# Optimization experiments

Measured on AMD Instinct MI355X. Metric: run time of the kernel, lower is better.

Reference implementation:

```python
import jax, jax.numpy as jnp
import numpy as np

N, E = 50000, 800000
IN, OUT, STEPS = 100, 200, 8
CAT = IN + OUT  # 300
EPS = 1e-5


def setup_inputs() -> dict:
    key = jax.random.key(0)
    ks = jax.random.split(key, 24)
    s = 0.05
    d = {}
    d["x"] = jax.random.normal(ks[0], (N, IN), jnp.float32)
    d["edge_index"] = jax.random.randint(ks[1], (2, E), 0, N, dtype=jnp.int32)
    # GatedGraphConv params: per-layer linear weight + shared GRUCell
    d["ggnn_w"] = jax.random.normal(ks[2], (STEPS, OUT, OUT), jnp.float32) * s
    d["gru_wih"] = jax.random.normal(ks[3], (3 * OUT, OUT), jnp.float32) * s
    d["gru_whh"] = jax.random.normal(ks[4], (3 * OUT, OUT), jnp.float32) * s
    d["gru_bih"] = jnp.zeros((3 * OUT,), jnp.float32)
    d["gru_bhh"] = jnp.zeros((3 * OUT,), jnp.float32)
    # conv branch on h_i (C=OUT)
    d["conv1_w"] = jax.random.normal(ks[5], (OUT, OUT, 4), jnp.float32) * s
    d["conv1_b"] = jnp.zeros((OUT,), jnp.float32)
    d["conv2_w"] = jax.random.normal(ks[6], (OUT, OUT, 2), jnp.float32) * s
    d["conv2_b"] = jnp.zeros((OUT,), jnp.float32)
    # conv branch on c_i (C=CAT)
    d["conv1c_w"] = jax.random.normal(ks[7], (CAT, CAT, 4), jnp.float32) * s
    d["conv1c_b"] = jnp.zeros((CAT,), jnp.float32)
    d["conv2c_w"] = jax.random.normal(ks[8], (CAT, CAT, 2), jnp.float32) * s
    d["conv2c_b"] = jnp.zeros((CAT,), jnp.float32)
    # batchnorms (training-mode batch stats; affine params)
    d["bn_g"] = jnp.ones((OUT,), jnp.float32)
    d["bn_b"] = jnp.zeros((OUT,), jnp.float32)
    d["bnc_g"] = jnp.ones((CAT,), jnp.float32)
    d["bnc_b"] = jnp.zeros((CAT,), jnp.float32)
    # output MLPs
    d["mlpy_w"] = jax.random.normal(ks[9], (2, OUT), jnp.float32) * s
    d["mlpy_b"] = jnp.zeros((2,), jnp.float32)
    d["mlpz_w"] = jax.random.normal(ks[10], (2, CAT), jnp.float32) * s
    d["mlpz_b"] = jnp.zeros((2,), jnp.float32)
    return d


def _batchnorm(x, g, b):  # x: [B, C, L], stats over (B, L) as in BN1d training
    mu = x.mean(axis=(0, 2), keepdims=True)
    var = ((x - mu) ** 2).mean(axis=(0, 2), keepdims=True)
    return (x - mu) / jnp.sqrt(var + EPS) * g[None, :, None] + b[None, :, None]


def _conv1d(x, w, b):  # x: [B, C, L], w: [O, I, K]
    y = jax.lax.conv_general_dilated(x, w, (1,), 'VALID',
                                     dimension_numbers=('NCH', 'OIH', 'NCH'))
    return y + b[None, :, None]


def _maxpool1d(x, k, s):  # x: [B, C, L]
    return jax.lax.reduce_window(x, -jnp.inf, jax.lax.max,
                                 (1, 1, k), (1, 1, s), 'VALID')


def _ggnn(x, edge_index, ggnn_w, gru_wih, gru_whh, gru_bih, gru_bhh):
    # PyG GatedGraphConv: pad features to out_channels, then per layer:
    # m = h @ W_l; agg[dst] += m[src]; h = GRUCell(agg, h)
    h = jnp.pad(x, ((0, 0), (0, OUT - IN)))  # [N, OUT]
    src, dst = edge_index[0], edge_index[1]

    def step(h, w):
        m = h @ w                                               # [N, OUT]
        agg = jax.ops.segment_sum(m[src], dst, num_segments=N)  # scatter-add
        gi = agg @ gru_wih.T + gru_bih
        gh = h @ gru_whh.T + gru_bhh
        ir, iz, ic = jnp.split(gi, 3, axis=1)
        hr, hz, hc = jnp.split(gh, 3, axis=1)
        r = jax.nn.sigmoid(ir + hr)
        z = jax.nn.sigmoid(iz + hz)
        n = jnp.tanh(ic + r * hc)
        return (1.0 - z) * n + z * h, None

    h, _ = jax.lax.scan(step, h, ggnn_w)
    return h


def reference(x, edge_index, ggnn_w, gru_wih, gru_whh, gru_bih, gru_bhh,
              conv1_w, conv1_b, conv2_w, conv2_b,
              conv1c_w, conv1c_b, conv2c_w, conv2c_b,
              bn_g, bn_b, bnc_g, bnc_b,
              mlpy_w, mlpy_b, mlpz_w, mlpz_b):
    h = _ggnn(x, edge_index, ggnn_w, gru_wih, gru_whh, gru_bih, gru_bhh)
    x_i = x[None]                      # [1, N, IN]
    h_i = h[None]                      # [1, N, OUT]
    c_i = jnp.concatenate([h_i, x_i], axis=-1)  # [1, N, CAT]

    y = jnp.transpose(h_i, (0, 2, 1))  # [1, OUT, N]
    y = _maxpool1d(jax.nn.relu(_batchnorm(_conv1d(y, conv1_w, conv1_b), bn_g, bn_b)), 4, 2)
    y = _maxpool1d(jax.nn.relu(_batchnorm(_conv1d(y, conv2_w, conv2_b), bn_g, bn_b)), 3, 2)
    Y2 = jnp.transpose(y, (0, 2, 1))   # [1, L2, OUT]

    zc = jnp.transpose(c_i, (0, 2, 1))  # [1, CAT, N]
    zc = _maxpool1d(jax.nn.relu(_batchnorm(_conv1d(zc, conv1c_w, conv1c_b), bnc_g, bnc_b)), 4, 2)
    zc = _maxpool1d(jax.nn.relu(_batchnorm(_conv1d(zc, conv2c_w, conv2c_b), bnc_g, bnc_b)), 3, 2)
    Z2 = jnp.transpose(zc, (0, 2, 1))  # [1, L2, CAT]

    before_avg = (Y2 @ mlpy_w.T + mlpy_b) * (Z2 @ mlpz_w.T + mlpz_b)  # [1, L2, 2]
    avg = before_avg.mean(axis=1)      # [1, 2]
    return jax.nn.softmax(avg, axis=-1)
```

## Files before the change

kernel.cpp:

```cpp
#include <hip/hip_runtime.h>
#include <cstdint>
#include <cstddef>

#define NNODES 50000
#define NEDGES 800000
#define FIN    100
#define FOUT   200
#define FCAT   300
#define NSTEPS 8
#define NSCANB 196

typedef unsigned short ushort_t;
typedef __bf16 bf16x8 __attribute__((ext_vector_type(8)));
typedef float  floatx4 __attribute__((ext_vector_type(4)));

__device__ __forceinline__ float bf2f(ushort_t u) {
  union { unsigned u; float f; } c; c.u = ((unsigned)u) << 16; return c.f;
}
__device__ __forceinline__ ushort_t f2bf(float f) {
  union { float f; unsigned u; } c; c.f = f;
  unsigned r = c.u + 0x7FFFu + ((c.u >> 16) & 1u);
  return (ushort_t)(r >> 16);
}
__device__ __forceinline__ float inval(const void* p, size_t i, int f32) {
  return f32 ? ((const float*)p)[i] : bf2f(((const ushort_t*)p)[i]);
}

__device__ __forceinline__ void gl2lds16(const ushort_t* g, ushort_t* l) {
  typedef const __attribute__((address_space(1))) unsigned int gu32;
  typedef __attribute__((address_space(3))) unsigned int lu32;
  __builtin_amdgcn_global_load_lds((gu32*)(uintptr_t)g, (lu32*)(uintptr_t)l, 16, 0, 0);
}

#define LOG2E 1.44269504f
__device__ __forceinline__ float fsigmoid(float x) {
  return __builtin_amdgcn_rcpf(1.f + __builtin_amdgcn_exp2f(-x * LOG2E));
}
__device__ __forceinline__ float ftanh(float a) {
  return 1.f - 2.f * __builtin_amdgcn_rcpf(1.f + __builtin_amdgcn_exp2f(2.f * LOG2E * a));
}

__global__ void probe_kernel(const void* xraw, int* flag) {
  const ushort_t* u = (const ushort_t*)xraw;
  int t = threadIdx.x;
  int bad = 0;
  for (int i = t; i < 2048; i += 64) {
    int e = (u[2 * i] >> 7) & 0xFF;
    if (e >= 0x88) bad++;
  }
  for (int off = 32; off; off >>= 1) bad += __shfl_down(bad, off);
  if (t == 0) *flag = (bad > 128) ? 1 : 0;
}

__global__ void zero_kernel(int* p, int n) {
  int i = blockIdx.x * 256 + threadIdx.x;
  if (i < n) p[i] = 0;
}

__global__ void sentinel_kernel(ushort_t* out) {
  if (threadIdx.x == 0 && blockIdx.x == 0) {
    out[0] = f2bf(0.123f);
    out[1] = f2bf(0.877f);
  }
}

__global__ void hinit_kernel(const void* __restrict__ x, const int* __restrict__ dflag,
                             ushort_t* __restrict__ h) {
  const int f32 = *dflag;
  int i = blockIdx.x * 256 + threadIdx.x;
  if (i >= NNODES * FOUT) return;
  int n = i / FOUT, c = i % FOUT;
  h[i] = (c < FIN) ? f2bf(inval(x, (size_t)n * FIN + c, f32)) : (ushort_t)0;
}

__global__ void ccat_kernel(const ushort_t* __restrict__ h, const void* __restrict__ x,
                            const int* __restrict__ dflag, ushort_t* __restrict__ cc) {
  const int f32 = *dflag;
  int i = blockIdx.x * 256 + threadIdx.x;
  if (i >= NNODES * FCAT) return;
  int n = i / FCAT, c = i % FCAT;
  cc[i] = (c < FOUT) ? h[n * FOUT + c] : f2bf(inval(x, (size_t)n * FIN + (c - FOUT), f32));
}

__global__ void hist_kernel(const int* __restrict__ dst, int* __restrict__ cnt) {
  int e = blockIdx.x * 256 + threadIdx.x;
  if (e < NEDGES) atomicAdd(&cnt[dst[e]], 1);
}

__global__ void bsum_kernel(const int* __restrict__ cnt, int* __restrict__ bsum) {
  __shared__ int red[4];
  int i = blockIdx.x * 256 + threadIdx.x;
  int v = (i < NNODES) ? cnt[i] : 0;
  for (int off = 32; off; off >>= 1) v += __shfl_down(v, off);
  int w = threadIdx.x >> 6;
  if ((threadIdx.x & 63) == 0) red[w] = v;
  __syncthreads();
  if (threadIdx.x == 0) bsum[blockIdx.x] = red[0] + red[1] + red[2] + red[3];
}

__global__ void bscan_kernel(const int* __restrict__ bsum, int* __restrict__ boff) {
  __shared__ int s[256];
  int t = threadIdx.x;
  int v = (t < NSCANB) ? bsum[t] : 0;
  s[t] = v;
  __syncthreads();
  for (int off = 1; off < 256; off <<= 1) {
    int u = (t >= off) ? s[t - off] : 0;
    __syncthreads();
    s[t] += u;
    __syncthreads();
  }
  if (t < NSCANB) boff[t] = s[t] - v;
}

__global__ void rowptr_kernel(const int* __restrict__ cnt, const int* __restrict__ boff,
                              int* __restrict__ row_ptr, int* __restrict__ cursor) {
  __shared__ int s[256];
  int t = threadIdx.x;
  int i = blockIdx.x * 256 + t;
  int v = (i < NNODES) ? cnt[i] : 0;
  s[t] = v;
  __syncthreads();
  for (int off = 1; off < 256; off <<= 1) {
    int u = (t >= off) ? s[t - off] : 0;
    __syncthreads();
    s[t] += u;
    __syncthreads();
  }
  if (i < NNODES) {
    int e = boff[blockIdx.x] + s[t] - v;
    row_ptr[i] = e; cursor[i] = e;
    if (i == NNODES - 1) row_ptr[NNODES] = boff[blockIdx.x] + s[t];
  }
}

__global__ void fill_kernel(const int* __restrict__ srcv, const int* __restrict__ dstv,
                            int* __restrict__ cursor, int* __restrict__ csr_src) {
  int e = blockIdx.x * 256 + threadIdx.x;
  if (e >= NEDGES) return;
  int p = atomicAdd(&cursor[dstv[e]], 1);
  csr_src[p] = srcv[e];
}

__global__ __launch_bounds__(256) void gather_kernel(
    const int* __restrict__ row_ptr, const int* __restrict__ csr_src,
    const ushort_t* __restrict__ h, ushort_t* __restrict__ Ag) {
  int g = threadIdx.x >> 6;
  int lane = threadIdx.x & 63;
  int n = blockIdx.x * 4 + g;
  if (n >= NNODES) return;
  if (lane >= 50) return;
  int s0 = row_ptr[n], s1 = row_ptr[n + 1];
  float a0 = 0.f, a1 = 0.f, a2 = 0.f, a3 = 0.f;
  int i = s0;
  for (; i + 3 < s1; i += 4) {
    int sa = csr_src[i], sb = csr_src[i + 1], sc = csr_src[i + 2], sd = csr_src[i + 3];
    ushort4 va = *(const ushort4*)&h[(size_t)sa * FOUT + lane * 4];
    ushort4 vb = *(const ushort4*)&h[(size_t)sb * FOUT + lane * 4];
    ushort4 vc = *(const ushort4*)&h[(size_t)sc * FOUT + lane * 4];
    ushort4 vd = *(const ushort4*)&h[(size_t)sd * FOUT + lane * 4];
    a0 += (bf2f(va.x) + bf2f(vb.x)) + (bf2f(vc.x) + bf2f(vd.x));
    a1 += (bf2f(va.y) + bf2f(vb.y)) + (bf2f(vc.y) + bf2f(vd.y));
    a2 += (bf2f(va.z) + bf2f(vb.z)) + (bf2f(vc.z) + bf2f(vd.z));
    a3 += (bf2f(va.w) + bf2f(vb.w)) + (bf2f(vc.w) + bf2f(vd.w));
  }
  for (; i < s1; i++) {
    int sa = csr_src[i];
    ushort4 va = *(const ushort4*)&h[(size_t)sa * FOUT + lane * 4];
    a0 += bf2f(va.x); a1 += bf2f(va.y); a2 += bf2f(va.z); a3 += bf2f(va.w);
  }
  ushort4 o;
  o.x = f2bf(a0); o.y = f2bf(a1); o.z = f2bf(a2); o.w = f2bf(a3);
  *(ushort4*)&Ag[(size_t)n * 400 + lane * 4] = o;
  *(ushort4*)&Ag[(size_t)n * 400 + FOUT + lane * 4] =
      *(const ushort4*)&h[(size_t)n * FOUT + lane * 4];
}

__global__ void pada_kernel(const void* __restrict__ src, const int* __restrict__ dflag,
                            ushort_t* __restrict__ dst, int K, int Kp, int rowsValid,
                            int total) {
  const int f32 = *dflag;
  int i = blockIdx.x * 256 + threadIdx.x;
  if (i >= total) return;
  int r = i / Kp, k = i % Kp;
  float v = (r < rowsValid && k < K) ? inval(src, (size_t)r * K + k, f32) : 0.f;
  dst[i] = f2bf(v);
}

__global__ void btgruq_kernel(const float* __restrict__ Wp, const void* __restrict__ whh,
                              const int* __restrict__ dflag, ushort_t* __restrict__ Bt) {
  const int f32 = *dflag;
  int i = blockIdx.x * 256 + threadIdx.x;
  if (i >= NSTEPS * 896 * 416) return;
  int l = i / (896 * 416);
  int rem = i % (896 * 416);
  int nn = rem / 416;
  int k = rem % 416;
  int c = nn >> 2, g = nn & 3;
  float v = 0.f;
  if (c < 200) {
    if (k < 200) {
      const float* wrow = Wp + ((size_t)l * 200 + k) * 600;
      if (g == 0) v = wrow[c];
      else if (g == 1) v = wrow[200 + c];
      else if (g == 2) v = wrow[400 + c];
    } else if (k < 400) {
      int kh = k - 200;
      if (g == 0) v = inval(whh, (size_t)c * 200 + kh, f32);
      else if (g == 1) v = inval(whh, (size_t)(200 + c) * 200 + kh, f32);
      else if (g == 3) v = inval(whh, (size_t)(400 + c) * 200 + kh, f32);
    }
  }
  Bt[((size_t)nn + 896 * (size_t)l) * 416 + k] = f2bf(v);
}

__global__ void btconv_kernel(const void* __restrict__ w, const int* __restrict__ dflag,
                              ushort_t* __restrict__ Bt, int C, int KT, int Kp,
                              int O, int total) {
  const int f32 = *dflag;
  int i = blockIdx.x * 256 + threadIdx.x;
  if (i >= total) return;
  int o = i / Kp, k = i % Kp;
  float v = 0.f;
  int K = C * KT;
  if (k < K && o < O) {
    int ktap = k / C; int ci = k % C;
    v = inval(w, ((size_t)o * C + ci) * KT + ktap, f32);
  }
  Bt[i] = f2bf(v);
}

__global__ void gbias_kernel(const void* __restrict__ bih, const void* __restrict__ bhh,
                             const int* __restrict__ dflag, float* __restrict__ gb) {
  const int f32 = *dflag;
  int c = blockIdx.x * 256 + threadIdx.x;
  if (c >= 200) return;
  gb[c]       = inval(bih, c, f32)       + inval(bhh, c, f32);
  gb[200 + c] = inval(bih, 200 + c, f32) + inval(bhh, 200 + c, f32);
  gb[400 + c] = inval(bih, 400 + c, f32);
  gb[600 + c] = inval(bhh, 400 + c, f32);
}

__device__ __forceinline__ bool xcd_tile(int id, int MT, int NT, int& mt, int& nt) {
  int xcd = id & 7;
  int slot = id >> 3;
  mt = xcd * ((MT + 7) >> 3) + slot / NT;
  nt = slot % NT;
  return mt < MT;
}

template <bool OUT_BF16>
__global__ __launch_bounds__(256) void gemm128(
    const ushort_t* __restrict__ A, int lda, const ushort_t* __restrict__ Bt,
    void* __restrict__ Cv, int ldc, int M, int N, int Kp,
    const float* __restrict__ bias) {
  __shared__ alignas(16) ushort_t As[128 * 32];
  __shared__ alignas(16) ushort_t Bs[128 * 32];
  const int MT = (M + 127) >> 7;
  const int NT = (N + 127) >> 7;
  int mt, nt;
  if (!xcd_tile(blockIdx.x, MT, NT, mt, nt)) return;
  const int m0 = mt * 128;
  const int n0 = nt * 128;
  const int tid = threadIdx.x;
  const int lane = tid & 63;
  const int wv = tid >> 6;
  const int wm = wv & 1;
  const int wn = wv >> 1;
  const int quad = lane >> 4;
  const int l15 = lane & 15;

  const int s0i = wv * 128 + lane;
  const int s1i = s0i + 64;
  const int r0 = s0i >> 2, c0 = (s0i & 3) ^ ((r0 >> 1) & 3);
  const int r1 = s1i >> 2, c1 = (s1i & 3) ^ ((r1 >> 1) & 3);
  int ar0 = m0 + r0; if (ar0 >= M) ar0 = M - 1;
  int ar1 = m0 + r1; if (ar1 >= M) ar1 = M - 1;
  const ushort_t* gA0 = A + (size_t)ar0 * lda + c0 * 8;
  const ushort_t* gA1 = A + (size_t)ar1 * lda + c1 * 8;
  const ushort_t* gB0 = Bt + (size_t)(n0 + r0) * Kp + c0 * 8;
  const ushort_t* gB1 = Bt + (size_t)(n0 + r1) * Kp + c1 * 8;
  ushort_t* lA0 = &As[(size_t)(wv * 128) * 8];
  ushort_t* lA1 = &As[(size_t)(wv * 128 + 64) * 8];
  ushort_t* lB0 = &Bs[(size_t)(wv * 128) * 8];
  ushort_t* lB1 = &Bs[(size_t)(wv * 128 + 64) * 8];

  floatx4 acc[4][4];
  #pragma unroll
  for (int a = 0; a < 4; a++)
    #pragma unroll
    for (int b = 0; b < 4; b++)
      acc[a][b] = (floatx4){0.f, 0.f, 0.f, 0.f};

  for (int k0 = 0; k0 < Kp; k0 += 32) {
    gl2lds16(gA0 + k0, lA0);
    gl2lds16(gA1 + k0, lA1);
    gl2lds16(gB0 + k0, lB0);
    gl2lds16(gB1 + k0, lB1);
    __syncthreads();
    bf16x8 af[4], bfr[4];
    #pragma unroll
    for (int t = 0; t < 4; t++) {
      int ra = wm * 64 + t * 16 + l15;
      int rb = wn * 64 + t * 16 + l15;
      af[t]  = *(const bf16x8*)&As[(ra * 4 + (quad ^ ((ra >> 1) & 3))) * 8];
      bfr[t] = *(const bf16x8*)&Bs[(rb * 4 + (quad ^ ((rb >> 1) & 3))) * 8];
    }
    #pragma unroll
    for (int tm = 0; tm < 4; tm++)
      #pragma unroll
      for (int tn = 0; tn < 4; tn++)
        acc[tm][tn] = __builtin_amdgcn_mfma_f32_16x16x32_bf16(af[tm], bfr[tn], acc[tm][tn], 0, 0, 0);
    __syncthreads();
  }

  #pragma unroll
  for (int tm = 0; tm < 4; tm++) {
    int row = m0 + wm * 64 + tm * 16 + quad * 4;
    #pragma unroll
    for (int tn = 0; tn < 4; tn++) {
      int col = n0 + wn * 64 + tn * 16 + l15;
      if (col < N) {
        float bb = bias ? bias[col] : 0.f;
        #pragma unroll
        for (int r = 0; r < 4; r++) {
          if (row + r < M) {
            float v = acc[tm][tn][r] + bb;
            if (OUT_BF16) ((ushort_t*)Cv)[(size_t)(row + r) * ldc + col] = f2bf(v);
            else          ((float*)Cv)[(size_t)(row + r) * ldc + col] = v;
          }
        }
      }
    }
  }
}

__global__ __launch_bounds__(256) void gemm_gru(
    const ushort_t* __restrict__ A, int lda, const ushort_t* __restrict__ Bt,
    ushort_t* __restrict__ h, int M, int Kp, const float* __restrict__ gb) {
  __shared__ alignas(16) ushort_t As[128 * 32];
  __shared__ alignas(16) ushort_t Bs[128 * 32];
  const int MT = (M + 127) >> 7;
  int mt, nt;
  if (!xcd_tile(blockIdx.x, MT, 7, mt, nt)) return;
  const int m0 = mt * 128;
  const int n0 = nt * 128;
  const int tid = threadIdx.x;
  const int lane = tid & 63;
  const int wv = tid >> 6;
  const int wm = wv & 1;
  const int wn = wv >> 1;
  const int quad = lane >> 4;
  const int l15 = lane & 15;

  const int s0i = wv * 128 + lane;
  const int s1i = s0i + 64;
  const int r0 = s0i >> 2, c0 = (s0i & 3) ^ ((r0 >> 1) & 3);
  const int r1 = s1i >> 2, c1 = (s1i & 3) ^ ((r1 >> 1) & 3);
  int ar0 = m0 + r0; if (ar0 >= M) ar0 = M - 1;
  int ar1 = m0 + r1; if (ar1 >= M) ar1 = M - 1;
  const ushort_t* gA0 = A + (size_t)ar0 * lda + c0 * 8;
  const ushort_t* gA1 = A + (size_t)ar1 * lda + c1 * 8;
  const ushort_t* gB0 = Bt + (size_t)(n0 + r0) * Kp + c0 * 8;
  const ushort_t* gB1 = Bt + (size_t)(n0 + r1) * Kp + c1 * 8;
  ushort_t* lA0 = &As[(size_t)(wv * 128) * 8];
  ushort_t* lA1 = &As[(size_t)(wv * 128 + 64) * 8];
  ushort_t* lB0 = &Bs[(size_t)(wv * 128) * 8];
  ushort_t* lB1 = &Bs[(size_t)(wv * 128 + 64) * 8];

  floatx4 acc[4][4];
  #pragma unroll
  for (int a = 0; a < 4; a++)
    #pragma unroll
    for (int b = 0; b < 4; b++)
      acc[a][b] = (floatx4){0.f, 0.f, 0.f, 0.f};

  for (int k0 = 0; k0 < Kp; k0 += 32) {
    gl2lds16(gA0 + k0, lA0);
    gl2lds16(gA1 + k0, lA1);
    gl2lds16(gB0 + k0, lB0);
    gl2lds16(gB1 + k0, lB1);
    __syncthreads();
    bf16x8 af[4], bfr[4];
    #pragma unroll
    for (int t = 0; t < 4; t++) {
      int ra = wm * 64 + t * 16 + l15;
      int rb = wn * 64 + t * 16 + l15;
      af[t]  = *(const bf16x8*)&As[(ra * 4 + (quad ^ ((ra >> 1) & 3))) * 8];
      bfr[t] = *(const bf16x8*)&Bs[(rb * 4 + (quad ^ ((rb >> 1) & 3))) * 8];
    }
    #pragma unroll
    for (int tm = 0; tm < 4; tm++)
      #pragma unroll
      for (int tn = 0; tn < 4; tn++)
        acc[tm][tn] = __builtin_amdgcn_mfma_f32_16x16x32_bf16(af[tm], bfr[tn], acc[tm][tn], 0, 0, 0);
    __syncthreads();
  }

  const int sb0 = l15 & 1;
  const int sb1 = (l15 >> 1) & 1;
  const int jch = l15 >> 2;
  const int chb = nt * 32 + wn * 16;
  #pragma unroll
  for (int tn = 0; tn < 4; tn++) {
    int chan = chb + tn * 4 + jch;
    bool chok = (chan < 200);
    float rb = 0.f, zb = 0.f, ib = 0.f, hb = 0.f;
    if (chok) {
      rb = gb[chan]; zb = gb[200 + chan]; ib = gb[400 + chan]; hb = gb[600 + chan];
    }
    #pragma unroll
    for (int tm = 0; tm < 4; tm++) {
      float v0 = acc[tm][tn][0], v1 = acc[tm][tn][1];
      float v2 = acc[tm][tn][2], v3 = acc[tm][tn][3];
      float t;
      t = __shfl_xor(sb0 ? v0 : v1, 1); if (sb0) v0 = t; else v1 = t;
      t = __shfl_xor(sb0 ? v2 : v3, 1); if (sb0) v2 = t; else v3 = t;
      t = __shfl_xor(sb1 ? v0 : v2, 2); if (sb1) v0 = t; else v2 = t;
      t = __shfl_xor(sb1 ? v1 : v3, 2); if (sb1) v1 = t; else v3 = t;
      int row = m0 + wm * 64 + tm * 16 + quad * 4 + (l15 & 3);
      if (row < M && chok) {
        float r_ = fsigmoid(v0 + rb);
        float z_ = fsigmoid(v1 + zb);
        float n_ = ftanh(v2 + ib + r_ * (v3 + hb));
        float ho = bf2f(h[(size_t)row * 200 + chan]);
        h[(size_t)row * 200 + chan] = f2bf((1.f - z_) * n_ + z_ * ho);
      }
    }
  }
}

__global__ void bias_kernel(const void* __restrict__ b, const int* __restrict__ dflag,
                            float* __restrict__ out, int n) {
  const int f32 = *dflag;
  int i = blockIdx.x * 256 + threadIdx.x;
  if (i < n) out[i] = inval(b, i, f32);
}

__global__ void stats_kernel(const float* __restrict__ X, int Lrows, int C,
                             float* __restrict__ sums, float* __restrict__ sumsq) {
  int r0 = blockIdx.x * 64;
  int rend = r0 + 64; if (rend > Lrows) rend = Lrows;
  for (int c = threadIdx.x; c < C; c += 256) {
    float s = 0.f, ss = 0.f;
    for (int r = r0; r < rend; r++) {
      float v = X[(size_t)r * C + c];
      s += v; ss += v * v;
    }
    atomicAdd(&sums[c], s);
    atomicAdd(&sumsq[c], ss);
  }
}

__global__ void bnpool_kernel(const float* __restrict__ X, int Lin, int C, int kk, int ss,
                              int Lp, const float* __restrict__ sums,
                              const float* __restrict__ sumsq,
                              const void* __restrict__ g, const void* __restrict__ b,
                              const int* __restrict__ dflag, ushort_t* __restrict__ out) {
  const int f32 = *dflag;
  int i = blockIdx.x * 256 + threadIdx.x;
  if (i >= Lp * C) return;
  int p = i / C, c = i % C;
  float inv = 1.f / (float)Lin;
  float mu = sums[c] * inv;
  float var = sumsq[c] * inv - mu * mu; if (var < 0.f) var = 0.f;
  float scale = inval(g, c, f32) * rsqrtf(var + 1e-5f);
  float shift = inval(b, c, f32) - mu * scale;
  float m = -1e30f;
  int base = p * ss;
  for (int r = 0; r < kk; r++) {
    float v = X[(size_t)(base + r) * C + c] * scale + shift;
    if (v > m) m = v;
  }
  if (m < 0.f) m = 0.f;
  out[(size_t)p * C + c] = f2bf(m);
}

__global__ __launch_bounds__(256) void final_kernel(
    const ushort_t* __restrict__ Y2, const ushort_t* __restrict__ Z2,
    const void* __restrict__ wy, const void* __restrict__ by,
    const void* __restrict__ wz, const void* __restrict__ bz,
    const int* __restrict__ dflag, float* __restrict__ pacc) {
  const int f32 = *dflag;
  __shared__ float bl[8];
  int g = threadIdx.x >> 6;
  int lane = threadIdx.x & 63;
  int row = blockIdx.x * 4 + g;
  float y0 = 0.f, y1 = 0.f, z0 = 0.f, z1 = 0.f;
  if (row < 12497) {
    for (int c = lane; c < 200; c += 64) {
      float v = bf2f(Y2[(size_t)row * 200 + c]);
      y0 += v * inval(wy, c, f32);
      y1 += v * inval(wy, 200 + c, f32);
    }
    for (int c = lane; c < 300; c += 64) {
      float v = bf2f(Z2[(size_t)row * 300 + c]);
      z0 += v * inval(wz, c, f32);
      z1 += v * inval(wz, 300 + c, f32);
    }
  }
  for (int off = 32; off > 0; off >>= 1) {
    y0 += __shfl_down(y0, off);
    y1 += __shfl_down(y1, off);
    z0 += __shfl_down(z0, off);
    z1 += __shfl_down(z1, off);
  }
  if (lane == 0) {
    float p0 = 0.f, p1 = 0.f;
    if (row < 12497) {
      p0 = (y0 + inval(by, 0, f32)) * (z0 + inval(bz, 0, f32));
      p1 = (y1 + inval(by, 1, f32)) * (z1 + inval(bz, 1, f32));
    }
    bl[g * 2] = p0; bl[g * 2 + 1] = p1;
  }
  __syncthreads();
  if (threadIdx.x == 0) {
    pacc[(size_t)blockIdx.x * 2]     = bl[0] + bl[2] + bl[4] + bl[6];
    pacc[(size_t)blockIdx.x * 2 + 1] = bl[1] + bl[3] + bl[5] + bl[7];
  }
}

__global__ __launch_bounds__(256) void finalize_kernel(
    const float* __restrict__ pacc, int nblk, const int* __restrict__ dflag,
    void* __restrict__ out) {
  const int f32 = *dflag;
  __shared__ float red[2][4];
  int t = threadIdx.x;
  float s0 = 0.f, s1 = 0.f;
  for (int i = t; i < nblk; i += 256) { s0 += pacc[2 * i]; s1 += pacc[2 * i + 1]; }
  for (int off = 32; off; off >>= 1) { s0 += __shfl_down(s0, off); s1 += __shfl_down(s1, off); }
  int w = t >> 6;
  if ((t & 63) == 0) { red[0][w] = s0; red[1][w] = s1; }
  __syncthreads();
  if (t == 0) {
    float a0 = (red[0][0] + red[0][1] + red[0][2] + red[0][3]) / 12497.f;
    float a1 = (red[1][0] + red[1][1] + red[1][2] + red[1][3]) / 12497.f;
    float mx = fmaxf(a0, a1);
    float e0 = expf(a0 - mx), e1 = expf(a1 - mx);
    float s = e0 + e1;
    if (f32) {
      ((float*)out)[0] = e0 / s;
      ((float*)out)[1] = e1 / s;
    } else {
      ((ushort_t*)out)[0] = f2bf(e0 / s);
      ((ushort_t*)out)[1] = f2bf(e1 / s);
    }
  }
}

static inline int xcd_grid(int M, int NT) {
  int MT = (M + 127) >> 7;
  int CH = (MT + 7) >> 3;
  return 8 * CH * NT;
}

extern "C" void kernel_launch(void* const* d_in, const int* in_sizes, int n_in,
                              void* d_out, int out_size, void* d_ws, size_t ws_size,
                              hipStream_t stream) {
  const void* x        = d_in[0];
  const int*  edge     = (const int*)d_in[1];
  const void* ggnn_w   = d_in[2];
  const void* gru_wih  = d_in[3];
  const void* gru_whh  = d_in[4];
  const void* gru_bih  = d_in[5];
  const void* gru_bhh  = d_in[6];
  const void* conv1_w  = d_in[7];
  const void* conv1_b  = d_in[8];
  const void* conv2_w  = d_in[9];
  const void* conv2_b  = d_in[10];
  const void* conv1c_w = d_in[11];
  const void* conv1c_b = d_in[12];
  const void* conv2c_w = d_in[13];
  const void* conv2c_b = d_in[14];
  const void* bn_g     = d_in[15];
  const void* bn_b     = d_in[16];
  const void* bnc_g    = d_in[17];
  const void* bnc_b    = d_in[18];
  const void* mlpy_w   = d_in[19];
  const void* mlpy_b   = d_in[20];
  const void* mlpz_w   = d_in[21];
  const void* mlpz_b   = d_in[22];
  const int* srcv = edge;
  const int* dstv = edge + NEDGES;

  char* p = (char*)d_ws;
  auto alloc = [&](size_t bytes) -> char* {
    char* r = p; p += (bytes + 255) & ~(size_t)255; return r;
  };
  ushort_t* h    = (ushort_t*)alloc(((size_t)NNODES * FOUT + 64) * 2);
  ushort_t* Ag   = (ushort_t*)alloc(((size_t)NNODES * 400 + 64) * 2);
  ushort_t* cc   = Ag;
  char*     R    = alloc((size_t)98 * 1000 * 1000);
  float*    C1   = (float*)R;
  float*    C2   = (float*)R;
  float*    C1c  = (float*)R;
  float*    C2c  = (float*)R;
  ushort_t* pooled1 = (ushort_t*)(R + 60000000);
  ushort_t* pooledc = (ushort_t*)(R + 70000000);
  ushort_t* Y2      = (ushort_t*)(R + 85000000);
  ushort_t* Z2      = (ushort_t*)(R + 90000000);
  ushort_t* BtG  = (ushort_t*)alloc((size_t)8 * 896 * 416 * 2);
  ushort_t* Bt1  = (ushort_t*)alloc((size_t)256 * 800 * 2);
  ushort_t* Bt2  = (ushort_t*)alloc((size_t)256 * 416 * 2);
  ushort_t* Bt1c = (ushort_t*)alloc((size_t)384 * 1216 * 2);
  ushort_t* Bt2c = (ushort_t*)alloc((size_t)384 * 608 * 2);
  ushort_t* gwp  = (ushort_t*)alloc((size_t)1600 * 224 * 2);
  ushort_t* wihp = (ushort_t*)alloc((size_t)640 * 224 * 2);
  float*    Wp   = (float*)alloc((size_t)1600 * 600 * 4);
  int*   csr_src = (int*)alloc((size_t)NEDGES * 4);
  int*   row_ptr = (int*)alloc((size_t)(NNODES + 1) * 4);
  int*   cursor  = (int*)alloc((size_t)NNODES * 4);
  int*   cnt     = (int*)alloc((size_t)NNODES * 4);
  int*   bsum    = (int*)alloc((size_t)(NSCANB + 4) * 4);
  int*   boff    = (int*)alloc((size_t)(NSCANB + 4) * 4);
  float* pacc    = (float*)alloc((size_t)3125 * 2 * 4);
  float* sb      = (float*)alloc((size_t)4300 * 4);
  float *s1 = sb, *ss1 = sb + 200, *s2 = sb + 400, *ss2 = sb + 600;
  float *sc1 = sb + 800, *ssc1 = sb + 1100, *sc2 = sb + 1400, *ssc2 = sb + 1700;
  int*   dflag = (int*)(sb + 2002);
  float* b1f   = sb + 2010;
  float* b2f   = sb + 2210;
  float* b1cf  = sb + 2410;
  float* b2cf  = sb + 2710;
  float* gb    = sb + 3100;

  size_t required = (size_t)(p - (char*)d_ws);
  if (required > ws_size) {
    sentinel_kernel<<<1, 64, 0, stream>>>((ushort_t*)d_out);
    return;
  }

  probe_kernel<<<1, 64, 0, stream>>>(x, dflag);
  zero_kernel<<<(NNODES + 255) / 256, 256, 0, stream>>>(cnt, NNODES);
  zero_kernel<<<(2000 + 255) / 256, 256, 0, stream>>>((int*)sb, 2000);
  hinit_kernel<<<(NNODES * FOUT + 255) / 256, 256, 0, stream>>>(x, dflag, h);

  pada_kernel<<<(1600 * 224 + 255) / 256, 256, 0, stream>>>(ggnn_w, dflag, gwp, 200, 224, 1600, 1600 * 224);
  pada_kernel<<<(640 * 224 + 255) / 256, 256, 0, stream>>>(gru_wih, dflag, wihp, 200, 224, 600, 640 * 224);
  gemm128<false><<<xcd_grid(1600, 5), 256, 0, stream>>>(gwp, 224, wihp, Wp, 600, 1600, 600, 224, nullptr);

  btgruq_kernel<<<(NSTEPS * 896 * 416 + 255) / 256, 256, 0, stream>>>(Wp, gru_whh, dflag, BtG);
  gbias_kernel<<<1, 256, 0, stream>>>(gru_bih, gru_bhh, dflag, gb);
  btconv_kernel<<<(256 * 800 + 255) / 256, 256, 0, stream>>>(conv1_w, dflag, Bt1, 200, 4, 800, 200, 256 * 800);
  btconv_kernel<<<(256 * 416 + 255) / 256, 256, 0, stream>>>(conv2_w, dflag, Bt2, 200, 2, 416, 200, 256 * 416);
  btconv_kernel<<<(384 * 1216 + 255) / 256, 256, 0, stream>>>(conv1c_w, dflag, Bt1c, 300, 4, 1216, 300, 384 * 1216);
  btconv_kernel<<<(384 * 608 + 255) / 256, 256, 0, stream>>>(conv2c_w, dflag, Bt2c, 300, 2, 608, 300, 384 * 608);
  bias_kernel<<<1, 256, 0, stream>>>(conv1_b, dflag, b1f, 200);
  bias_kernel<<<1, 256, 0, stream>>>(conv2_b, dflag, b2f, 200);
  bias_kernel<<<2, 256, 0, stream>>>(conv1c_b, dflag, b1cf, 300);
  bias_kernel<<<2, 256, 0, stream>>>(conv2c_b, dflag, b2cf, 300);

  hist_kernel<<<(NEDGES + 255) / 256, 256, 0, stream>>>(dstv, cnt);
  bsum_kernel<<<NSCANB, 256, 0, stream>>>(cnt, bsum);
  bscan_kernel<<<1, 256, 0, stream>>>(bsum, boff);
  rowptr_kernel<<<NSCANB, 256, 0, stream>>>(cnt, boff, row_ptr, cursor);
  fill_kernel<<<(NEDGES + 255) / 256, 256, 0, stream>>>(srcv, dstv, cursor, csr_src);

  for (int l = 0; l < NSTEPS; l++) {
    gather_kernel<<<(NNODES + 3) / 4, 256, 0, stream>>>(row_ptr, csr_src, h, Ag);
    gemm_gru<<<xcd_grid(NNODES, 7), 256, 0, stream>>>(Ag, 400, BtG + (size_t)l * 896 * 416,
                                                      h, NNODES, 416, gb);
  }
  ccat_kernel<<<(NNODES * FCAT + 255) / 256, 256, 0, stream>>>(h, x, dflag, cc);

  gemm128<false><<<xcd_grid(49997, 2), 256, 0, stream>>>(h, 200, Bt1, C1, 200, 49997, 200, 800, b1f);
  stats_kernel<<<(49997 + 63) / 64, 256, 0, stream>>>(C1, 49997, 200, s1, ss1);
  bnpool_kernel<<<(24997 * 200 + 255) / 256, 256, 0, stream>>>(C1, 49997, 200, 4, 2, 24997,
                                                               s1, ss1, bn_g, bn_b, dflag, pooled1);
  gemm128<false><<<xcd_grid(24996, 2), 256, 0, stream>>>(pooled1, 200, Bt2, C2, 200, 24996, 200, 416, b2f);
  stats_kernel<<<(24996 + 63) / 64, 256, 0, stream>>>(C2, 24996, 200, s2, ss2);
  bnpool_kernel<<<(12497 * 200 + 255) / 256, 256, 0, stream>>>(C2, 24996, 200, 3, 2, 12497,
                                                               s2, ss2, bn_g, bn_b, dflag, Y2);
  gemm128<false><<<xcd_grid(49997, 3), 256, 0, stream>>>(cc, 300, Bt1c, C1c, 300, 49997, 300, 1216, b1cf);
  stats_kernel<<<(49997 + 63) / 64, 256, 0, stream>>>(C1c, 49997, 300, sc1, ssc1);
  bnpool_kernel<<<(24997 * 300 + 255) / 256, 256, 0, stream>>>(C1c, 49997, 300, 4, 2, 24997,
                                                               sc1, ssc1, bnc_g, bnc_b, dflag, pooledc);
  gemm128<false><<<xcd_grid(24996, 3), 256, 0, stream>>>(pooledc, 300, Bt2c, C2c, 300, 24996, 300, 608, b2cf);
  stats_kernel<<<(24996 + 63) / 64, 256, 0, stream>>>(C2c, 24996, 300, sc2, ssc2);
  bnpool_kernel<<<(12497 * 300 + 255) / 256, 256, 0, stream>>>(C2c, 24996, 300, 3, 2, 12497,
                                                               sc2, ssc2, bnc_g, bnc_b, dflag, Z2);

  final_kernel<<<3125, 256, 0, stream>>>(Y2, Z2, mlpy_w, mlpy_b, mlpz_w, mlpz_b, dflag, pacc);
  finalize_kernel<<<1, 256, 0, stream>>>(pacc, 3125, dflag, d_out);
}
```

Before: 1.797 ms.

## Fuse BN statistics into conv GEMM epilogue and drop h copy in gather

```diff
diff --git a/kernel.cpp b/kernel.cpp
--- a/kernel.cpp
+++ b/kernel.cpp
@@ -144,7 +144,7 @@
 
 __global__ __launch_bounds__(256) void gather_kernel(
     const int* __restrict__ row_ptr, const int* __restrict__ csr_src,
-    const ushort_t* __restrict__ h, ushort_t* __restrict__ Ag) {
+    const ushort_t* __restrict__ h, ushort_t* __restrict__ agg) {
   int g = threadIdx.x >> 6;
   int lane = threadIdx.x & 63;
   int n = blockIdx.x * 4 + g;
@@ -171,9 +171,7 @@
   }
   ushort4 o;
   o.x = f2bf(a0); o.y = f2bf(a1); o.z = f2bf(a2); o.w = f2bf(a3);
-  *(ushort4*)&Ag[(size_t)n * 400 + lane * 4] = o;
-  *(ushort4*)&Ag[(size_t)n * 400 + FOUT + lane * 4] =
-      *(const ushort4*)&h[(size_t)n * FOUT + lane * 4];
+  *(ushort4*)&agg[(size_t)n * 224 + lane * 4] = o;
 }
 
 __global__ void pada_kernel(const void* __restrict__ src, const int* __restrict__ dflag,
@@ -191,11 +189,11 @@
                               const int* __restrict__ dflag, ushort_t* __restrict__ Bt) {
   const int f32 = *dflag;
   int i = blockIdx.x * 256 + threadIdx.x;
-  if (i >= NSTEPS * 896 * 416) return;
-  int l = i / (896 * 416);
-  int rem = i % (896 * 416);
-  int nn = rem / 416;
-  int k = rem % 416;
+  if (i >= NSTEPS * 896 * 448) return;
+  int l = i / (896 * 448);
+  int rem = i % (896 * 448);
+  int nn = rem / 448;
+  int k = rem % 448;
   int c = nn >> 2, g = nn & 3;
   float v = 0.f;
   if (c < 200) {
@@ -204,14 +202,14 @@
       if (g == 0) v = wrow[c];
       else if (g == 1) v = wrow[200 + c];
       else if (g == 2) v = wrow[400 + c];
-    } else if (k < 400) {
-      int kh = k - 200;
+    } else if (k >= 224 && k < 424) {
+      int kh = k - 224;
       if (g == 0) v = inval(whh, (size_t)c * 200 + kh, f32);
       else if (g == 1) v = inval(whh, (size_t)(200 + c) * 200 + kh, f32);
       else if (g == 3) v = inval(whh, (size_t)(400 + c) * 200 + kh, f32);
     }
   }
-  Bt[((size_t)nn + 896 * (size_t)l) * 416 + k] = f2bf(v);
+  Bt[((size_t)nn + 896 * (size_t)l) * 448 + k] = f2bf(v);
 }
 
 __global__ void btconv_kernel(const void* __restrict__ w, const int* __restrict__ dflag,
@@ -335,9 +333,128 @@
   }
 }
 
+__global__ __launch_bounds__(256) void gemm_conv(
+    const ushort_t* __restrict__ A, int lda, const ushort_t* __restrict__ Bt,
+    ushort_t* __restrict__ C, int ldc, int M, int N, int Kp,
+    const float* __restrict__ bias, float* __restrict__ partS, float* __restrict__ partQ) {
+  __shared__ alignas(16) ushort_t As[128 * 32];
+  __shared__ alignas(16) ushort_t Bs[128 * 32];
+  const int MT = (M + 127) >> 7;
+  const int NT = (N + 127) >> 7;
+  int mt, nt;
+  if (!xcd_tile(blockIdx.x, MT, NT, mt, nt)) return;
+  const int m0 = mt * 128;
+  const int n0 = nt * 128;
+  const int tid = threadIdx.x;
+  const int lane = tid & 63;
+  const int wv = tid >> 6;
+  const int wm = wv & 1;
+  const int wn = wv >> 1;
+  const int quad = lane >> 4;
+  const int l15 = lane & 15;
+
+  const int s0i = wv * 128 + lane;
+  const int s1i = s0i + 64;
+  const int r0 = s0i >> 2, c0 = (s0i & 3) ^ ((r0 >> 1) & 3);
+  const int r1 = s1i >> 2, c1 = (s1i & 3) ^ ((r1 >> 1) & 3);
+  int ar0 = m0 + r0; if (ar0 >= M) ar0 = M - 1;
+  int ar1 = m0 + r1; if (ar1 >= M) ar1 = M - 1;
+  const ushort_t* gA0 = A + (size_t)ar0 * lda + c0 * 8;
+  const ushort_t* gA1 = A + (size_t)ar1 * lda + c1 * 8;
+  const ushort_t* gB0 = Bt + (size_t)(n0 + r0) * Kp + c0 * 8;
+  const ushort_t* gB1 = Bt + (size_t)(n0 + r1) * Kp + c1 * 8;
+  ushort_t* lA0 = &As[(size_t)(wv * 128) * 8];
+  ushort_t* lA1 = &As[(size_t)(wv * 128 + 64) * 8];
+  ushort_t* lB0 = &Bs[(size_t)(wv * 128) * 8];
+  ushort_t* lB1 = &Bs[(size_t)(wv * 128 + 64) * 8];
+
+  floatx4 acc[4][4];
+  #pragma unroll
+  for (int a = 0; a < 4; a++)
+    #pragma unroll
+    for (int b = 0; b < 4; b++)
+      acc[a][b] = (floatx4){0.f, 0.f, 0.f, 0.f};
+
+  for (int k0 = 0; k0 < Kp; k0 += 32) {
+    gl2lds16(gA0 + k0, lA0);
+    gl2lds16(gA1 + k0, lA1);
+    gl2lds16(gB0 + k0, lB0);
+    gl2lds16(gB1 + k0, lB1);
+    __syncthreads();
+    bf16x8 af[4], bfr[4];
+    #pragma unroll
+    for (int t = 0; t < 4; t++) {
+      int ra = wm * 64 + t * 16 + l15;
+      int rb = wn * 64 + t * 16 + l15;
+      af[t]  = *(const bf16x8*)&As[(ra * 4 + (quad ^ ((ra >> 1) & 3))) * 8];
+      bfr[t] = *(const bf16x8*)&Bs[(rb * 4 + (quad ^ ((rb >> 1) & 3))) * 8];
+    }
+    #pragma unroll
+    for (int tm = 0; tm < 4; tm++)
+      #pragma unroll
+      for (int tn = 0; tn < 4; tn++)
+        acc[tm][tn] = __builtin_amdgcn_mfma_f32_16x16x32_bf16(af[tm], bfr[tn], acc[tm][tn], 0, 0, 0);
+    __syncthreads();
+  }
+
+  float sS[4], sQ[4];
+  #pragma unroll
+  for (int tn = 0; tn < 4; tn++) {
+    int col = n0 + wn * 64 + tn * 16 + l15;
+    float bb = (col < N) ? bias[col] : 0.f;
+    float s = 0.f, q = 0.f;
+    #pragma unroll
+    for (int tm = 0; tm < 4; tm++) {
+      int row = m0 + wm * 64 + tm * 16 + quad * 4;
+      #pragma unroll
+      for (int r = 0; r < 4; r++) {
+        if (row + r < M) {
+          float v = acc[tm][tn][r] + bb;
+          if (col < N) C[(size_t)(row + r) * ldc + col] = f2bf(v);
+          s += v; q += v * v;
+        }
+      }
+    }
+    s += __shfl_down(s, 32); s += __shfl_down(s, 16);
+    q += __shfl_down(q, 32); q += __shfl_down(q, 16);
+    sS[tn] = s; sQ[tn] = q;
+  }
+  float* pS = (float*)As;
+  float* pQ = (float*)Bs;
+  if (quad == 0) {
+    #pragma unroll
+    for (int tn = 0; tn < 4; tn++) {
+      pS[wv * 64 + tn * 16 + l15] = sS[tn];
+      pQ[wv * 64 + tn * 16 + l15] = sQ[tn];
+    }
+  }
+  __syncthreads();
+  if (tid < 128) {
+    int wnc = tid >> 6, off = tid & 63;
+    int col = n0 + tid;
+    if (col < N) {
+      partS[(size_t)mt * N + col] = pS[(2 * wnc) * 64 + off] + pS[(2 * wnc + 1) * 64 + off];
+      partQ[(size_t)mt * N + col] = pQ[(2 * wnc) * 64 + off] + pQ[(2 * wnc + 1) * 64 + off];
+    }
+  }
+}
+
+__global__ void statred_kernel(const float* __restrict__ partS, const float* __restrict__ partQ,
+                               int MT, int N, float* __restrict__ sums, float* __restrict__ sumsq) {
+  int c = blockIdx.x * 256 + threadIdx.x;
+  if (c >= N) return;
+  float s = 0.f, q = 0.f;
+  for (int m = 0; m < MT; m++) {
+    s += partS[(size_t)m * N + c];
+    q += partQ[(size_t)m * N + c];
+  }
+  sums[c] = s; sumsq[c] = q;
+}
+
 __global__ __launch_bounds__(256) void gemm_gru(
-    const ushort_t* __restrict__ A, int lda, const ushort_t* __restrict__ Bt,
-    ushort_t* __restrict__ h, int M, int Kp, const float* __restrict__ gb) {
+    const ushort_t* __restrict__ agg, const ushort_t* __restrict__ hin,
+    const ushort_t* __restrict__ Bt, ushort_t* __restrict__ hout,
+    int M, const float* __restrict__ gb) {
   __shared__ alignas(16) ushort_t As[128 * 32];
   __shared__ alignas(16) ushort_t Bs[128 * 32];
   const int MT = (M + 127) >> 7;
@@ -359,10 +476,12 @@
   const int r1 = s1i >> 2, c1 = (s1i & 3) ^ ((r1 >> 1) & 3);
   int ar0 = m0 + r0; if (ar0 >= M) ar0 = M - 1;
   int ar1 = m0 + r1; if (ar1 >= M) ar1 = M - 1;
-  const ushort_t* gA0 = A + (size_t)ar0 * lda + c0 * 8;
-  const ushort_t* gA1 = A + (size_t)ar1 * lda + c1 * 8;
-  const ushort_t* gB0 = Bt + (size_t)(n0 + r0) * Kp + c0 * 8;
-  const ushort_t* gB1 = Bt + (size_t)(n0 + r1) * Kp + c1 * 8;
+  const ushort_t* gAg0 = agg + (size_t)ar0 * 224 + c0 * 8;
+  const ushort_t* gAg1 = agg + (size_t)ar1 * 224 + c1 * 8;
+  const ushort_t* gAh0 = hin + (size_t)ar0 * 200 + c0 * 8;
+  const ushort_t* gAh1 = hin + (size_t)ar1 * 200 + c1 * 8;
+  const ushort_t* gB0 = Bt + (size_t)(n0 + r0) * 448 + c0 * 8;
+  const ushort_t* gB1 = Bt + (size_t)(n0 + r1) * 448 + c1 * 8;
   ushort_t* lA0 = &As[(size_t)(wv * 128) * 8];
   ushort_t* lA1 = &As[(size_t)(wv * 128 + 64) * 8];
   ushort_t* lB0 = &Bs[(size_t)(wv * 128) * 8];
@@ -375,9 +494,11 @@
     for (int b = 0; b < 4; b++)
       acc[a][b] = (floatx4){0.f, 0.f, 0.f, 0.f};
 
-  for (int k0 = 0; k0 < Kp; k0 += 32) {
-    gl2lds16(gA0 + k0, lA0);
-    gl2lds16(gA1 + k0, lA1);
+  for (int k0 = 0; k0 < 448; k0 += 32) {
+    const ushort_t* a0 = (k0 < 224) ? (gAg0 + k0) : (gAh0 + (k0 - 224));
+    const ushort_t* a1 = (k0 < 224) ? (gAg1 + k0) : (gAh1 + (k0 - 224));
+    gl2lds16(a0, lA0);
+    gl2lds16(a1, lA1);
     gl2lds16(gB0 + k0, lB0);
     gl2lds16(gB1 + k0, lB1);
     __syncthreads();
@@ -423,8 +544,8 @@
         float r_ = fsigmoid(v0 + rb);
         float z_ = fsigmoid(v1 + zb);
         float n_ = ftanh(v2 + ib + r_ * (v3 + hb));
-        float ho = bf2f(h[(size_t)row * 200 + chan]);
-        h[(size_t)row * 200 + chan] = f2bf((1.f - z_) * n_ + z_ * ho);
+        float ho = bf2f(hin[(size_t)row * 200 + chan]);
+        hout[(size_t)row * 200 + chan] = f2bf((1.f - z_) * n_ + z_ * ho);
       }
     }
   }
@@ -437,22 +558,7 @@
   if (i < n) out[i] = inval(b, i, f32);
 }
 
-__global__ void stats_kernel(const float* __restrict__ X, int Lrows, int C,
-                             float* __restrict__ sums, float* __restrict__ sumsq) {
-  int r0 = blockIdx.x * 64;
-  int rend = r0 + 64; if (rend > Lrows) rend = Lrows;
-  for (int c = threadIdx.x; c < C; c += 256) {
-    float s = 0.f, ss = 0.f;
-    for (int r = r0; r < rend; r++) {
-      float v = X[(size_t)r * C + c];
-      s += v; ss += v * v;
-    }
-    atomicAdd(&sums[c], s);
-    atomicAdd(&sumsq[c], ss);
-  }
-}
-
-__global__ void bnpool_kernel(const float* __restrict__ X, int Lin, int C, int kk, int ss,
+__global__ void bnpool_kernel(const ushort_t* __restrict__ X, int Lin, int C, int kk, int ss,
                               int Lp, const float* __restrict__ sums,
                               const float* __restrict__ sumsq,
                               const void* __restrict__ g, const void* __restrict__ b,
@@ -469,7 +575,7 @@
   float m = -1e30f;
   int base = p * ss;
   for (int r = 0; r < kk; r++) {
-    float v = X[(size_t)(base + r) * C + c] * scale + shift;
+    float v = bf2f(X[(size_t)(base + r) * C + c]) * scale + shift;
     if (v > m) m = v;
   }
   if (m < 0.f) m = 0.f;
@@ -588,18 +694,19 @@
     char* r = p; p += (bytes + 255) & ~(size_t)255; return r;
   };
   ushort_t* h    = (ushort_t*)alloc(((size_t)NNODES * FOUT + 64) * 2);
+  ushort_t* h1   = (ushort_t*)alloc(((size_t)NNODES * FOUT + 64) * 2);
   ushort_t* Ag   = (ushort_t*)alloc(((size_t)NNODES * 400 + 64) * 2);
   ushort_t* cc   = Ag;
   char*     R    = alloc((size_t)98 * 1000 * 1000);
-  float*    C1   = (float*)R;
-  float*    C2   = (float*)R;
-  float*    C1c  = (float*)R;
-  float*    C2c  = (float*)R;
+  ushort_t* C1b  = (ushort_t*)R;
+  ushort_t* C2b  = (ushort_t*)R;
+  ushort_t* C1cb = (ushort_t*)R;
+  ushort_t* C2cb = (ushort_t*)R;
   ushort_t* pooled1 = (ushort_t*)(R + 60000000);
   ushort_t* pooledc = (ushort_t*)(R + 70000000);
   ushort_t* Y2      = (ushort_t*)(R + 85000000);
   ushort_t* Z2      = (ushort_t*)(R + 90000000);
-  ushort_t* BtG  = (ushort_t*)alloc((size_t)8 * 896 * 416 * 2);
+  ushort_t* BtG  = (ushort_t*)alloc((size_t)8 * 896 * 448 * 2);
   ushort_t* Bt1  = (ushort_t*)alloc((size_t)256 * 800 * 2);
   ushort_t* Bt2  = (ushort_t*)alloc((size_t)256 * 416 * 2);
   ushort_t* Bt1c = (ushort_t*)alloc((size_t)384 * 1216 * 2);
@@ -607,6 +714,8 @@
   ushort_t* gwp  = (ushort_t*)alloc((size_t)1600 * 224 * 2);
   ushort_t* wihp = (ushort_t*)alloc((size_t)640 * 224 * 2);
   float*    Wp   = (float*)alloc((size_t)1600 * 600 * 4);
+  float*    partS = (float*)alloc((size_t)391 * 300 * 4);
+  float*    partQ = (float*)alloc((size_t)391 * 300 * 4);
   int*   csr_src = (int*)alloc((size_t)NEDGES * 4);
   int*   row_ptr = (int*)alloc((size_t)(NNODES + 1) * 4);
   int*   cursor  = (int*)alloc((size_t)NNODES * 4);
@@ -639,7 +748,7 @@
   pada_kernel<<<(640 * 224 + 255) / 256, 256, 0, stream>>>(gru_wih, dflag, wihp, 200, 224, 600, 640 * 224);
   gemm128<false><<<xcd_grid(1600, 5), 256, 0, stream>>>(gwp, 224, wihp, Wp, 600, 1600, 600, 224, nullptr);
 
-  btgruq_kernel<<<(NSTEPS * 896 * 416 + 255) / 256, 256, 0, stream>>>(Wp, gru_whh, dflag, BtG);
+  btgruq_kernel<<<(NSTEPS * 896 * 448 + 255) / 256, 256, 0, stream>>>(Wp, gru_whh, dflag, BtG);
   gbias_kernel<<<1, 256, 0, stream>>>(gru_bih, gru_bhh, dflag, gb);
   btconv_kernel<<<(256 * 800 + 255) / 256, 256, 0, stream>>>(conv1_w, dflag, Bt1, 200, 4, 800, 200, 256 * 800);
   btconv_kernel<<<(256 * 416 + 255) / 256, 256, 0, stream>>>(conv2_w, dflag, Bt2, 200, 2, 416, 200, 256 * 416);
@@ -656,28 +765,35 @@
   rowptr_kernel<<<NSCANB, 256, 0, stream>>>(cnt, boff, row_ptr, cursor);
   fill_kernel<<<(NEDGES + 255) / 256, 256, 0, stream>>>(srcv, dstv, cursor, csr_src);
 
+  ushort_t* hcur = h;
+  ushort_t* hnxt = h1;
   for (int l = 0; l < NSTEPS; l++) {
-    gather_kernel<<<(NNODES + 3) / 4, 256, 0, stream>>>(row_ptr, csr_src, h, Ag);
-    gemm_gru<<<xcd_grid(NNODES, 7), 256, 0, stream>>>(Ag, 400, BtG + (size_t)l * 896 * 416,
-                                                      h, NNODES, 416, gb);
+    gather_kernel<<<(NNODES + 3) / 4, 256, 0, stream>>>(row_ptr, csr_src, hcur, Ag);
+    gemm_gru<<<xcd_grid(NNODES, 7), 256, 0, stream>>>(Ag, hcur, BtG + (size_t)l * 896 * 448,
+                                                      hnxt, NNODES, gb);
+    ushort_t* tmp = hcur; hcur = hnxt; hnxt = tmp;
   }
   ccat_kernel<<<(NNODES * FCAT + 255) / 256, 256, 0, stream>>>(h, x, dflag, cc);
 
-  gemm128<false><<<xcd_grid(49997, 2), 256, 0, stream>>>(h, 200, Bt1, C1, 200, 49997, 200, 800, b1f);
-  stats_kernel<<<(49997 + 63) / 64, 256, 0, stream>>>(C1, 49997, 200, s1, ss1);
-  bnpool_kernel<<<(24997 * 200 + 255) / 256, 256, 0, stream>>>(C1, 49997, 200, 4, 2, 24997,
+  gemm_conv<<<xcd_grid(49997, 2), 256, 0, stream>>>(h, 200, Bt1, C1b, 200, 49997, 200, 800,
+                                                    b1f, partS, partQ);
+  statred_kernel<<<1, 256, 0, stream>>>(partS, partQ, 391, 200, s1, ss1);
+  bnpool_kernel<<<(24997 * 200 + 255) / 256, 256, 0, stream>>>(C1b, 49997, 200, 4, 2, 24997,
                                                                s1, ss1, bn_g, bn_b, dflag, pooled1);
-  gemm128<false><<<xcd_grid(24996, 2), 256, 0, stream>>>(pooled1, 200, Bt2, C2, 200, 24996, 200, 416, b2f);
-  stats_kernel<<<(24996 + 63) / 64, 256, 0, stream>>>(C2, 24996, 200, s2, ss2);
-  bnpool_kernel<<<(12497 * 200 + 255) / 256, 256, 0, stream>>>(C2, 24996, 200, 3, 2, 12497,
+  gemm_conv<<<xcd_grid(24996, 2), 256, 0, stream>>>(pooled1, 200, Bt2, C2b, 200, 24996, 200, 416,
+                                                    b2f, partS, partQ);
+  statred_kernel<<<1, 256, 0, stream>>>(partS, partQ, 196, 200, s2, ss2);
+  bnpool_kernel<<<(12497 * 200 + 255) / 256, 256, 0, stream>>>(C2b, 24996, 200, 3, 2, 12497,
                                                                s2, ss2, bn_g, bn_b, dflag, Y2);
-  gemm128<false><<<xcd_grid(49997, 3), 256, 0, stream>>>(cc, 300, Bt1c, C1c, 300, 49997, 300, 1216, b1cf);
-  stats_kernel<<<(49997 + 63) / 64, 256, 0, stream>>>(C1c, 49997, 300, sc1, ssc1);
-  bnpool_kernel<<<(24997 * 300 + 255) / 256, 256, 0, stream>>>(C1c, 49997, 300, 4, 2, 24997,
+  gemm_conv<<<xcd_grid(49997, 3), 256, 0, stream>>>(cc, 300, Bt1c, C1cb, 300, 49997, 300, 1216,
+                                                    b1cf, partS, partQ);
+  statred_kernel<<<2, 256, 0, stream>>>(partS, partQ, 391, 300, sc1, ssc1);
+  bnpool_kernel<<<(24997 * 300 + 255) / 256, 256, 0, stream>>>(C1cb, 49997, 300, 4, 2, 24997,
                                                                sc1, ssc1, bnc_g, bnc_b, dflag, pooledc);
-  gemm128<false><<<xcd_grid(24996, 3), 256, 0, stream>>>(pooledc, 300, Bt2c, C2c, 300, 24996, 300, 608, b2cf);
-  stats_kernel<<<(24996 + 63) / 64, 256, 0, stream>>>(C2c, 24996, 300, sc2, ssc2);
-  bnpool_kernel<<<(12497 * 300 + 255) / 256, 256, 0, stream>>>(C2c, 24996, 300, 3, 2, 12497,
+  gemm_conv<<<xcd_grid(24996, 3), 256, 0, stream>>>(pooledc, 300, Bt2c, C2cb, 300, 24996, 300, 608,
+                                                    b2cf, partS, partQ);
+  statred_kernel<<<2, 256, 0, stream>>>(partS, partQ, 196, 300, sc2, ssc2);
+  bnpool_kernel<<<(12497 * 300 + 255) / 256, 256, 0, stream>>>(C2cb, 24996, 300, 3, 2, 12497,
                                                                sc2, ssc2, bnc_g, bnc_b, dflag, Z2);
 
   final_kernel<<<3125, 256, 0, stream>>>(Y2, Z2, mlpy_w, mlpy_b, mlpz_w, mlpz_b, dflag, pacc);
```

New measurement: 1.891 ms. 5.2% more time.
